# Kernel optimization log

Hardware: AMD Instinct MI355X
Metric: run time of the kernel (lower is better)

## Reference

```python
import jax, jax.numpy as jnp
import numpy as np

D = 768
H = 12
EPS = 1e-5


def layer_norm(x, g, b):
    mu = jnp.mean(x, axis=-1, keepdims=True)
    var = jnp.var(x, axis=-1, keepdims=True)
    return (x - mu) * jax.lax.rsqrt(var + EPS) * g + b


def setup_inputs() -> dict:
    key = jax.random.key(0)
    ks = jax.random.split(key, 12)
    d, h = D, H
    x = jax.random.normal(ks[0], (4, 1024, d), dtype=jnp.float32)
    # attention projections (per-head dim is full d, per the module)
    s_qkv = (6.0 / (d + d * h)) ** 0.5  # xavier-like scale
    Wq = jax.random.uniform(ks[1], (d, d * h), jnp.float32, -s_qkv, s_qkv)
    Wk = jax.random.uniform(ks[2], (d, d * h), jnp.float32, -s_qkv, s_qkv)
    Wv = jax.random.uniform(ks[3], (d, d * h), jnp.float32, -s_qkv, s_qkv)
    Wu = jax.random.uniform(ks[4], (d * h, d), jnp.float32, -s_qkv, s_qkv)
    bu = jnp.zeros((d,), jnp.float32)
    # MLP
    s1 = (6.0 / (d + 4 * d)) ** 0.5
    W1 = jax.random.uniform(ks[5], (d, 4 * d), jnp.float32, -s1, s1)
    b1 = jax.random.normal(ks[6], (4 * d,), jnp.float32) * 1e-6
    W2 = jax.random.uniform(ks[7], (4 * d, d), jnp.float32, -s1, s1)
    b2 = jax.random.normal(ks[8], (d,), jnp.float32) * 1e-6
    ln1_g = jnp.ones((d,), jnp.float32)
    ln1_b = jnp.zeros((d,), jnp.float32)
    ln2_g = jnp.ones((d,), jnp.float32)
    ln2_b = jnp.zeros((d,), jnp.float32)
    return dict(x=x, Wq=Wq, Wk=Wk, Wv=Wv, Wu=Wu, bu=bu,
                ln1_g=ln1_g, ln1_b=ln1_b, ln2_g=ln2_g, ln2_b=ln2_b,
                W1=W1, b1=b1, W2=W2, b2=b2)


def reference(x, Wq, Wk, Wv, Wu, bu, ln1_g, ln1_b, ln2_g, ln2_b, W1, b1, W2, b2):
    b, n, d = x.shape
    h = H
    # --- pre-LN attention block ---
    res = x
    y = layer_norm(x, ln1_g, ln1_b)
    qs = (y @ Wq).reshape(b, n, h, d)  # per-head dim = d (module quirk)
    ks = (y @ Wk).reshape(b, n, h, d)
    vs = (y @ Wv).reshape(b, n, h, d)
    scores = jnp.einsum('bihd,bjhd->bhij', qs, ks) / (d ** 0.5)
    w = jax.nn.softmax(scores, axis=-1)
    att = jnp.einsum('bhij,bjhd->bihd', w, vs).reshape(b, n, h * d)
    y = att @ Wu + bu
    x = y + res
    # --- pre-LN MLP block (dropout is identity at inference) ---
    res = x
    y = layer_norm(x, ln2_g, ln2_b)
    y = jax.nn.relu(y @ W1 + b1)
    y = y @ W2 + b2
    return y + res
```

## Files before the change

kernel.cpp:

```cpp
#include <hip/hip_runtime.h>
#include <cstdint>
#include <cmath>


typedef __bf16 bf16_t;
typedef __bf16 bf16x8 __attribute__((ext_vector_type(8)));
typedef __bf16 bf16x4 __attribute__((ext_vector_type(4)));
typedef float floatx4 __attribute__((ext_vector_type(4)));

#define DMODEL 768
#define NHEAD  12
#define SEQ    1024
#define NBATCH 4
#define ROWS   (NBATCH*SEQ)
#define DH     (DMODEL*NHEAD)
#define DFF    (4*DMODEL)

template<bool BIAS, bool RES, bool RELU, int OMODE>
__global__ __launch_bounds__(256)
void gemm_v7(const bf16_t* __restrict__ A, const bf16_t* __restrict__ BT,
             void* __restrict__ Cv, int K, int lda, int ldb, int ldc,
             int bdiv, long sa_hi, long sa_lo, long sb_hi, long sb_lo,
             long sc_hi, long sc_lo,
             const float* __restrict__ bias, const float* __restrict__ res,
             int ldres, float alpha)
{
  __shared__ __align__(16) bf16_t As[128*64];
  __shared__ __align__(16) bf16_t Bs[128*64];

  const int tid  = threadIdx.x;
  const int wave = tid >> 6;
  const int lane = tid & 63;
  const int r    = lane & 15;
  const int q    = lane >> 4;

  const int z = blockIdx.z;
  A  += (long)(z / bdiv) * sa_hi + (long)(z % bdiv) * sa_lo;
  BT += (long)(z / bdiv) * sb_hi + (long)(z % bdiv) * sb_lo;
  const long coff = (long)(z / bdiv) * sc_hi + (long)(z % bdiv) * sc_lo;

  const int bm = blockIdx.y * 128;
  const int bn = blockIdx.x * 128;
  const int wm = (wave & 1) * 64;
  const int wn = (wave >> 1) * 64;

  const int blk0 = 2*wave, blk1 = 2*wave + 1;
  const bf16_t* a_src0 = A  + (long)(bm + blk0*16 + r) * lda + q*8;
  const bf16_t* a_src1 = A  + (long)(bm + blk1*16 + r) * lda + q*8;
  const bf16_t* b_src0 = BT + (long)(bn + blk0*16 + r) * ldb + q*8;
  const bf16_t* b_src1 = BT + (long)(bn + blk1*16 + r) * ldb + q*8;
  const int da0 = blk0*512 + lane*8;
  const int da1 = blk1*512 + lane*8;

  const int am = (wave & 1) * 4;
  const int bb = (wave >> 1) * 4;

  floatx4 acc[4][4] = {};

  for (int k0 = 0; k0 < K; k0 += 64) {
    bf16x8 a00 = *(const bf16x8*)(a_src0 + k0);
    bf16x8 a01 = *(const bf16x8*)(a_src0 + k0 + 32);
    bf16x8 a10 = *(const bf16x8*)(a_src1 + k0);
    bf16x8 a11 = *(const bf16x8*)(a_src1 + k0 + 32);
    bf16x8 b00 = *(const bf16x8*)(b_src0 + k0);
    bf16x8 b01 = *(const bf16x8*)(b_src0 + k0 + 32);
    bf16x8 b10 = *(const bf16x8*)(b_src1 + k0);
    bf16x8 b11 = *(const bf16x8*)(b_src1 + k0 + 32);
    *(bf16x8*)(As + da0)        = a00;
    *(bf16x8*)(As + 4096 + da0) = a01;
    *(bf16x8*)(As + da1)        = a10;
    *(bf16x8*)(As + 4096 + da1) = a11;
    *(bf16x8*)(Bs + da0)        = b00;
    *(bf16x8*)(Bs + 4096 + da0) = b01;
    *(bf16x8*)(Bs + da1)        = b10;
    *(bf16x8*)(Bs + 4096 + da1) = b11;
    __syncthreads();
#pragma unroll
    for (int p = 0; p < 2; ++p) {
      bf16x8 afrag[4], bfrag[4];
#pragma unroll
      for (int t = 0; t < 4; ++t) {
        afrag[t] = *(const bf16x8*)(As + p*4096 + (am + t)*512 + lane*8);
        bfrag[t] = *(const bf16x8*)(Bs + p*4096 + (bb + t)*512 + lane*8);
      }
#pragma unroll
      for (int mt = 0; mt < 4; ++mt)
#pragma unroll
        for (int nt = 0; nt < 4; ++nt)
          acc[mt][nt] = __builtin_amdgcn_mfma_f32_16x16x32_bf16(
              afrag[mt], bfrag[nt], acc[mt][nt], 0, 0, 0);
    }
    __syncthreads();
  }

  const int row0 = bm + wm + q*4;
  const int col0 = bn + wn + r;
#pragma unroll
  for (int nt = 0; nt < 4; ++nt) {
    const int col = col0 + nt*16;
    float bv = 0.f;
    if (BIAS) bv = bias[col];
#pragma unroll
    for (int mt = 0; mt < 4; ++mt) {
#pragma unroll
      for (int e = 0; e < 4; ++e) {
        const int rowi = row0 + mt*16 + e;
        float v = acc[mt][nt][e] * alpha;
        if (BIAS) v += bv;
        if (RELU) v = fmaxf(v, 0.f);
        if (RES)  v += res[(long)rowi * ldres + col];
        const long idx = coff + (long)rowi * ldc + col;
        if (OMODE == 0)      ((bf16_t*)Cv)[idx] = (bf16_t)v;
        else if (OMODE == 1) ((float*)Cv)[idx] = v;
        else                 ((float*)Cv)[idx] += v;
      }
    }
  }
}

__global__ void tr_f2b_v7(const float* __restrict__ in, bf16_t* __restrict__ out,
                          int ldi, int ldo)
{
  __shared__ bf16_t tile[32][34];
  const int c0 = blockIdx.x * 32, r0 = blockIdx.y * 32;
  const int tx = threadIdx.x, ty = threadIdx.y;
#pragma unroll
  for (int i = 0; i < 4; ++i)
    tile[ty + 8*i][tx] = (bf16_t)in[(long)(r0 + ty + 8*i) * ldi + c0 + tx];
  __syncthreads();
#pragma unroll
  for (int i = 0; i < 4; ++i)
    out[(long)(c0 + ty + 8*i) * ldo + r0 + tx] = tile[tx][ty + 8*i];
}

__global__ void tr_b_v7(const bf16_t* __restrict__ in, bf16_t* __restrict__ out,
                        int ldi, int ldo, int bdiv,
                        long si_hi, long si_lo, long so_hi, long so_lo)
{
  __shared__ bf16_t tile[32][34];
  const int z = blockIdx.z;
  in  += (long)(z / bdiv) * si_hi + (long)(z % bdiv) * si_lo;
  out += (long)(z / bdiv) * so_hi + (long)(z % bdiv) * so_lo;
  const int c0 = blockIdx.x * 32, r0 = blockIdx.y * 32;
  const int tx = threadIdx.x, ty = threadIdx.y;
#pragma unroll
  for (int i = 0; i < 4; ++i)
    tile[ty + 8*i][tx] = in[(long)(r0 + ty + 8*i) * ldi + c0 + tx];
  __syncthreads();
#pragma unroll
  for (int i = 0; i < 4; ++i)
    out[(long)(c0 + ty + 8*i) * ldo + r0 + tx] = tile[tx][ty + 8*i];
}

__global__ void tr_wh_v7(const float* __restrict__ Wq, const float* __restrict__ Wk,
                         const float* __restrict__ Wv, const float* __restrict__ Wu,
                         bf16_t* __restrict__ WhT, bf16_t* __restrict__ WuTh, int h)
{
  __shared__ bf16_t tile[32][34];
  const int z = blockIdx.z;
  const float* in; bf16_t* out; int ldi;
  if (z < 3) {
    const float* W = (z == 0) ? Wq : (z == 1) ? Wk : Wv;
    in  = W + (long)h * DMODEL;
    ldi = DH;
    out = WhT + (long)z * DMODEL * DMODEL;
  } else {
    in  = Wu + (long)h * DMODEL * DMODEL;
    ldi = DMODEL;
    out = WuTh;
  }
  const int c0 = blockIdx.x * 32, r0 = blockIdx.y * 32;
  const int tx = threadIdx.x, ty = threadIdx.y;
#pragma unroll
  for (int i = 0; i < 4; ++i)
    tile[ty + 8*i][tx] = (bf16_t)in[(long)(r0 + ty + 8*i) * ldi + c0 + tx];
  __syncthreads();
#pragma unroll
  for (int i = 0; i < 4; ++i)
    out[(long)(c0 + ty + 8*i) * DMODEL + r0 + tx] = tile[tx][ty + 8*i];
}

__global__ void cast3_v7(const float* __restrict__ a, const float* __restrict__ b,
                         const float* __restrict__ c,
                         bf16_t* __restrict__ oa, bf16_t* __restrict__ ob,
                         bf16_t* __restrict__ oc)
{
  const float* src = (blockIdx.z == 0) ? a : (blockIdx.z == 1) ? b : c;
  bf16_t* dst      = (blockIdx.z == 0) ? oa : (blockIdx.z == 1) ? ob : oc;
  const long i = ((long)blockIdx.x * 256 + threadIdx.x) * 4;
  float4 v = *(const float4*)(src + i);
  bf16x4 o;
  o[0] = (bf16_t)v.x; o[1] = (bf16_t)v.y; o[2] = (bf16_t)v.z; o[3] = (bf16_t)v.w;
  *(bf16x4*)(dst + i) = o;
}

__global__ void cast1_v7(const float* __restrict__ src, bf16_t* __restrict__ dst)
{
  const long i = ((long)blockIdx.x * 256 + threadIdx.x) * 4;
  float4 v = *(const float4*)(src + i);
  bf16x4 o;
  o[0] = (bf16_t)v.x; o[1] = (bf16_t)v.y; o[2] = (bf16_t)v.z; o[3] = (bf16_t)v.w;
  *(bf16x4*)(dst + i) = o;
}

__global__ void ln_v7(const float* __restrict__ x, const float* __restrict__ g,
                      const float* __restrict__ b, bf16_t* __restrict__ y)
{
  const long row = blockIdx.x;
  const int tid = threadIdx.x;
  const float* xr = x + row * DMODEL;
  float v0 = xr[tid], v1 = xr[tid + 256], v2 = xr[tid + 512];
  float s  = v0 + v1 + v2;
  float ss = v0*v0 + v1*v1 + v2*v2;
  for (int o = 32; o; o >>= 1) { s += __shfl_down(s, o); ss += __shfl_down(ss, o); }
  __shared__ float rs[4], rss[4];
  const int wave = tid >> 6, lane = tid & 63;
  if (lane == 0) { rs[wave] = s; rss[wave] = ss; }
  __syncthreads();
  s  = rs[0] + rs[1] + rs[2] + rs[3];
  ss = rss[0] + rss[1] + rss[2] + rss[3];
  const float inv = 1.0f / (float)DMODEL;
  const float mean = s * inv;
  const float var  = ss * inv - mean * mean;
  const float rstd = rsqrtf(var + 1e-5f);
  bf16_t* yr = y + row * DMODEL;
  yr[tid]       = (bf16_t)(((v0 - mean) * rstd) * g[tid]       + b[tid]);
  yr[tid + 256] = (bf16_t)(((v1 - mean) * rstd) * g[tid + 256] + b[tid + 256]);
  yr[tid + 512] = (bf16_t)(((v2 - mean) * rstd) * g[tid + 512] + b[tid + 512]);
}

__global__ void softmax_v7(bf16_t* __restrict__ S)
{
  const long row = blockIdx.x;
  const int tid = threadIdx.x;
  bf16_t* p = S + row * SEQ + tid * 4;
  bf16x4 v = *(const bf16x4*)p;
  float f0 = (float)v[0], f1 = (float)v[1], f2 = (float)v[2], f3 = (float)v[3];
  float m = fmaxf(fmaxf(f0, f1), fmaxf(f2, f3));
  for (int o = 32; o; o >>= 1) m = fmaxf(m, __shfl_down(m, o));
  __shared__ float rm[4], rsum[4];
  const int wave = tid >> 6, lane = tid & 63;
  if (lane == 0) rm[wave] = m;
  __syncthreads();
  m = fmaxf(fmaxf(rm[0], rm[1]), fmaxf(rm[2], rm[3]));
  float e0 = __expf(f0 - m), e1 = __expf(f1 - m), e2 = __expf(f2 - m), e3 = __expf(f3 - m);
  float s = e0 + e1 + e2 + e3;
  for (int o = 32; o; o >>= 1) s += __shfl_down(s, o);
  if (lane == 0) rsum[wave] = s;
  __syncthreads();
  s = rsum[0] + rsum[1] + rsum[2] + rsum[3];
  const float invs = 1.0f / s;
  bf16x4 o4;
  o4[0] = (bf16_t)(e0 * invs); o4[1] = (bf16_t)(e1 * invs);
  o4[2] = (bf16_t)(e2 * invs); o4[3] = (bf16_t)(e3 * invs);
  *(bf16x4*)p = o4;
}

__global__ void finalize_v7(const float* __restrict__ acc, const float* __restrict__ add,
                            const float* __restrict__ bias, float* __restrict__ o)
{
  const long i = (long)blockIdx.x * 256 + threadIdx.x;
  const int c = (int)(i % DMODEL);
  o[i] = acc[i] + bias[c] + add[i];
}

template<int NP>
__global__ void reduce_v7(const float* __restrict__ p, const float* __restrict__ add,
                          const float* __restrict__ bias, float* __restrict__ o,
                          long plane)
{
  const long i = ((long)blockIdx.x * 256 + threadIdx.x) * 4;
  float4 s = *(const float4*)(p + i);
#pragma unroll
  for (int n = 1; n < NP; ++n) {
    float4 v = *(const float4*)(p + i + (long)n * plane);
    s.x += v.x; s.y += v.y; s.z += v.z; s.w += v.w;
  }
  const int c = (int)(i % DMODEL);
  float4 bv = *(const float4*)(bias + c);
  float4 av = *(const float4*)(add + i);
  float4 r;
  r.x = s.x + bv.x + av.x; r.y = s.y + bv.y + av.y;
  r.z = s.z + bv.z + av.z; r.w = s.w + bv.w + av.w;
  *(float4*)(o + i) = r;
}

extern "C" void kernel_launch(void* const* d_in, const int* in_sizes, int n_in,
                              void* d_out, int out_size, void* d_ws, size_t ws_size,
                              hipStream_t stream)
{
  (void)in_sizes; (void)n_in; (void)out_size;
  const float* x    = (const float*)d_in[0];
  const float* Wq   = (const float*)d_in[1];
  const float* Wk   = (const float*)d_in[2];
  const float* Wv   = (const float*)d_in[3];
  const float* Wu   = (const float*)d_in[4];
  const float* bu   = (const float*)d_in[5];
  const float* ln1g = (const float*)d_in[6];
  const float* ln1b = (const float*)d_in[7];
  const float* ln2g = (const float*)d_in[8];
  const float* ln2b = (const float*)d_in[9];
  const float* W1   = (const float*)d_in[10];
  const float* b1   = (const float*)d_in[11];
  const float* W2   = (const float*)d_in[12];
  const float* b2   = (const float*)d_in[13];
  float* out = (float*)d_out;

  char* ws = (char*)d_ws;
  size_t off = 0;
  auto alloc = [&](size_t bytes) -> void* {
    void* p = (void*)(ws + off);
    off += (bytes + 255) & ~(size_t)255;
    return p;
  };

  const float qk_alpha = 1.0f / sqrtf((float)DMODEL);
  dim3 tb(32, 8);

  const size_t SZ_W   = (size_t)DMODEL * DH * 2;
  const size_t SZ_MT  = (size_t)NHEAD * DMODEL * DMODEL * 2;
  const size_t SZ_Y   = (size_t)ROWS * DMODEL * 2;
  const size_t SZ_X2  = (size_t)ROWS * DMODEL * 4;

  if (ws_size >= (size_t)262e6) {
    bf16_t* MT   = (bf16_t*)alloc(SZ_MT);
    bf16_t* PhT  = (bf16_t*)alloc(SZ_MT);
    bf16_t* y    = (bf16_t*)alloc(SZ_Y);
    float*  x2f  = (float* )alloc(SZ_X2);
    float*  part = (float* )alloc((size_t)3 * ROWS * DMODEL * 4);
    bf16_t* S    = (bf16_t*)alloc((size_t)NBATCH * SEQ * NHEAD * SEQ * 2);
    bf16_t* Zt   = (bf16_t*)alloc((size_t)NBATCH * DMODEL * NHEAD * SEQ * 2);
    bf16_t* T_b  = (bf16_t*)part;
    bf16_t* Wqb  = (bf16_t*)S;
    bf16_t* Wkb  = (bf16_t*)((char*)S + SZ_W);
    bf16_t* Wvb  = (bf16_t*)((char*)S + 2*SZ_W);
    bf16_t* WuT  = (bf16_t*)((char*)S + 3*SZ_W);
    bf16_t* W1T  = (bf16_t*)S;
    bf16_t* W2T  = (bf16_t*)((char*)S + 4718592);
    bf16_t* t    = (bf16_t*)((char*)S + 9437184);
    float*  partM= (float* )((char*)S + 34603008);
    bf16_t* y2   = (bf16_t*)Zt;

    cast3_v7<<<dim3(6912, 1, 3), 256, 0, stream>>>(Wq, Wk, Wv, Wqb, Wkb, Wvb);
    tr_f2b_v7<<<dim3(DMODEL/32, DH/32), tb, 0, stream>>>(Wu, WuT, DMODEL, DH);
    gemm_v7<false,false,false,0><<<dim3(6, 6, NHEAD), 256, 0, stream>>>(
        Wkb, Wqb, MT, DMODEL, DH, DH, DMODEL, NHEAD,
        0, DMODEL, 0, DMODEL, 0, (long)DMODEL*DMODEL, nullptr, nullptr, 0, 1.0f);
    gemm_v7<false,false,false,0><<<dim3(6, 6, NHEAD), 256, 0, stream>>>(
        WuT, Wvb, PhT, DMODEL, DH, DH, DMODEL, NHEAD,
        0, DMODEL, 0, DMODEL, 0, (long)DMODEL*DMODEL, nullptr, nullptr, 0, 1.0f);

    ln_v7<<<ROWS, 256, 0, stream>>>(x, ln1g, ln1b, y);
    for (int b = 0; b < NBATCH; ++b) {
      const bf16_t* yb = y + (long)b * SEQ * DMODEL;
      gemm_v7<false,false,false,0><<<dim3(6, 8, NHEAD), 256, 0, stream>>>(
          yb, MT, T_b, DMODEL, DMODEL, DMODEL, DMODEL, NHEAD,
          0, 0, 0, (long)DMODEL*DMODEL, 0, (long)SEQ*DMODEL,
          nullptr, nullptr, 0, 1.0f);
      gemm_v7<false,false,false,0><<<dim3(8, 8, NHEAD), 256, 0, stream>>>(
          T_b, yb, S + (long)b*SEQ*NHEAD*SEQ, DMODEL, DMODEL, DMODEL, NHEAD*SEQ, NHEAD,
          0, (long)SEQ*DMODEL, 0, 0, 0, (long)SEQ,
          nullptr, nullptr, 0, qk_alpha);
    }
    softmax_v7<<<NBATCH*SEQ*NHEAD, 256, 0, stream>>>(S);
    gemm_v7<false,false,false,0><<<dim3(8, 6, NBATCH*NHEAD), 256, 0, stream>>>(
        PhT, y, Zt, DMODEL, DMODEL, DMODEL, NHEAD*SEQ, NHEAD,
        0, (long)DMODEL*DMODEL, (long)SEQ*DMODEL, 0,
        (long)DMODEL*NHEAD*SEQ, (long)SEQ, nullptr, nullptr, 0, 1.0f);
    gemm_v7<false,false,false,1><<<dim3(6, 8, 12), 256, 0, stream>>>(
        S, Zt, part, NHEAD*SEQ/3, NHEAD*SEQ, NHEAD*SEQ, DMODEL, NBATCH,
        (long)(NHEAD*SEQ/3), (long)SEQ*NHEAD*SEQ,
        (long)(NHEAD*SEQ/3), (long)DMODEL*NHEAD*SEQ,
        (long)ROWS*DMODEL, (long)SEQ*DMODEL, nullptr, nullptr, 0, 1.0f);
    reduce_v7<3><<<(ROWS*DMODEL)/1024, 256, 0, stream>>>(
        part, x, bu, x2f, (long)ROWS*DMODEL);

    tr_f2b_v7<<<dim3(DFF/32, DMODEL/32), tb, 0, stream>>>(W1, W1T, DFF, DMODEL);
    tr_f2b_v7<<<dim3(DMODEL/32, DFF/32), tb, 0, stream>>>(W2, W2T, DMODEL, DFF);
    ln_v7<<<ROWS, 256, 0, stream>>>(x2f, ln2g, ln2b, y2);
    gemm_v7<true,false,true,0><<<dim3(DFF/128, ROWS/128, 1), 256, 0, stream>>>(
        y2, W1T, t, DMODEL, DMODEL, DMODEL, DFF, 1, 0,0,0,0,0,0, b1, nullptr, 0, 1.0f);
    gemm_v7<false,false,false,1><<<dim3(6, ROWS/128, 4), 256, 0, stream>>>(
        t, W2T, partM, DFF/4, DFF, DFF, DMODEL, 4,
        0, (long)(DFF/4), 0, (long)(DFF/4), 0, (long)ROWS*DMODEL,
        nullptr, nullptr, 0, 1.0f);
    reduce_v7<4><<<(ROWS*DMODEL)/1024, 256, 0, stream>>>(
        partM, x2f, b2, out, (long)ROWS*DMODEL);
  } else if (ws_size >= (size_t)112e6) {
    bf16_t* MT  = (bf16_t*)alloc(SZ_MT);
    bf16_t* PhT = (bf16_t*)alloc(SZ_MT);
    bf16_t* y   = (bf16_t*)alloc(SZ_Y);
    float*  x2f = (float* )alloc(SZ_X2);
    char*   BIG = (char*  )alloc((size_t)62914560);
    bf16_t* T_b  = (bf16_t*)(BIG);
    bf16_t* S_b  = (bf16_t*)(BIG + 18874368);
    bf16_t* Zt_b = (bf16_t*)(BIG + 44040192);
    float*  part = (float* )(BIG);
    bf16_t* Wqb = (bf16_t*)(BIG);
    bf16_t* Wkb = (bf16_t*)(BIG + SZ_W);
    bf16_t* Wvb = (bf16_t*)(BIG + 2*SZ_W);
    bf16_t* WuT = (bf16_t*)(BIG + 3*SZ_W);
    bf16_t* W1T   = (bf16_t*)(BIG);
    bf16_t* W2T   = (bf16_t*)(BIG + 4718592);
    bf16_t* t     = (bf16_t*)(BIG + 9437184);
    float*  partM = (float* )(BIG + 34603008);
    bf16_t* y2    = y;

    cast3_v7<<<dim3(6912, 1, 3), 256, 0, stream>>>(Wq, Wk, Wv, Wqb, Wkb, Wvb);
    tr_f2b_v7<<<dim3(DMODEL/32, DH/32), tb, 0, stream>>>(Wu, WuT, DMODEL, DH);
    gemm_v7<false,false,false,0><<<dim3(6, 6, NHEAD), 256, 0, stream>>>(
        Wkb, Wqb, MT, DMODEL, DH, DH, DMODEL, NHEAD,
        0, DMODEL, 0, DMODEL, 0, (long)DMODEL*DMODEL, nullptr, nullptr, 0, 1.0f);
    gemm_v7<false,false,false,0><<<dim3(6, 6, NHEAD), 256, 0, stream>>>(
        WuT, Wvb, PhT, DMODEL, DH, DH, DMODEL, NHEAD,
        0, DMODEL, 0, DMODEL, 0, (long)DMODEL*DMODEL, nullptr, nullptr, 0, 1.0f);

    ln_v7<<<ROWS, 256, 0, stream>>>(x, ln1g, ln1b, y);
    for (int b = 0; b < NBATCH; ++b) {
      const bf16_t* yb = y + (long)b * SEQ * DMODEL;
      gemm_v7<false,false,false,0><<<dim3(6, 8, NHEAD), 256, 0, stream>>>(
          yb, MT, T_b, DMODEL, DMODEL, DMODEL, DMODEL, NHEAD,
          0, 0, 0, (long)DMODEL*DMODEL, 0, (long)SEQ*DMODEL,
          nullptr, nullptr, 0, 1.0f);
      gemm_v7<false,false,false,0><<<dim3(8, 8, NHEAD), 256, 0, stream>>>(
          T_b, yb, S_b, DMODEL, DMODEL, DMODEL, NHEAD*SEQ, NHEAD,
          0, (long)SEQ*DMODEL, 0, 0, 0, (long)SEQ,
          nullptr, nullptr, 0, qk_alpha);
      softmax_v7<<<NHEAD*SEQ, 256, 0, stream>>>(S_b);
      gemm_v7<false,false,false,0><<<dim3(8, 6, NHEAD), 256, 0, stream>>>(
          PhT, yb, Zt_b, DMODEL, DMODEL, DMODEL, NHEAD*SEQ, NHEAD,
          0, (long)DMODEL*DMODEL, 0, 0, 0, (long)SEQ,
          nullptr, nullptr, 0, 1.0f);
      gemm_v7<false,false,false,1><<<dim3(6, 8, 6), 256, 0, stream>>>(
          S_b, Zt_b, part, NHEAD*SEQ/6, NHEAD*SEQ, NHEAD*SEQ, DMODEL, 6,
          0, (long)(NHEAD*SEQ/6), 0, (long)(NHEAD*SEQ/6), 0, (long)SEQ*DMODEL,
          nullptr, nullptr, 0, 1.0f);
      reduce_v7<6><<<(SEQ*DMODEL)/1024, 256, 0, stream>>>(
          part, x + (long)b*SEQ*DMODEL, bu, x2f + (long)b*SEQ*DMODEL,
          (long)SEQ*DMODEL);
    }

    tr_f2b_v7<<<dim3(DFF/32, DMODEL/32), tb, 0, stream>>>(W1, W1T, DFF, DMODEL);
    tr_f2b_v7<<<dim3(DMODEL/32, DFF/32), tb, 0, stream>>>(W2, W2T, DMODEL, DFF);
    ln_v7<<<ROWS, 256, 0, stream>>>(x2f, ln2g, ln2b, y2);
    gemm_v7<true,false,true,0><<<dim3(DFF/128, ROWS/128, 1), 256, 0, stream>>>(
        y2, W1T, t, DMODEL, DMODEL, DMODEL, DFF, 1, 0,0,0,0,0,0, b1, nullptr, 0, 1.0f);
    gemm_v7<false,false,false,1><<<dim3(6, ROWS/128, 2), 256, 0, stream>>>(
        t, W2T, partM, DFF/2, DFF, DFF, DMODEL, 2,
        0, (long)(DFF/2), 0, (long)(DFF/2), 0, (long)ROWS*DMODEL,
        nullptr, nullptr, 0, 1.0f);
    reduce_v7<2><<<(ROWS*DMODEL)/1024, 256, 0, stream>>>(
        partM, x2f, b2, out, (long)ROWS*DMODEL);
  } else if (ws_size >= (size_t)70e6) {
    bf16_t* MT  = (bf16_t*)alloc(SZ_MT);
    bf16_t* PhT = (bf16_t*)alloc(SZ_MT);
    bf16_t* y   = (bf16_t*)alloc(SZ_Y);
    char*   R   = (char*  )alloc((size_t)33554432);
    bf16_t* WAb = (bf16_t*)(R);
    bf16_t* WBb = (bf16_t*)(R + SZ_W);
    float*  x2f = (float* )(R);
    bf16_t* T_h = (bf16_t*)(R + 12582912);
    bf16_t* S_h = (bf16_t*)(R + 18874368);
    bf16_t* Z_h = (bf16_t*)(R + 27262976);
    bf16_t* W1T = (bf16_t*)(R + 12582912);
    bf16_t* W2T = (bf16_t*)(R + 17301504);
    bf16_t* t   = (bf16_t*)MT;
    bf16_t* y2  = y;

    cast1_v7<<<6912, 256, 0, stream>>>(Wq, WAb);
    cast1_v7<<<6912, 256, 0, stream>>>(Wk, WBb);
    gemm_v7<false,false,false,0><<<dim3(6, 6, NHEAD), 256, 0, stream>>>(
        WBb, WAb, MT, DMODEL, DH, DH, DMODEL, NHEAD,
        0, DMODEL, 0, DMODEL, 0, (long)DMODEL*DMODEL, nullptr, nullptr, 0, 1.0f);
    cast1_v7<<<6912, 256, 0, stream>>>(Wv, WAb);
    tr_f2b_v7<<<dim3(DMODEL/32, DH/32), tb, 0, stream>>>(Wu, WBb, DMODEL, DH);
    gemm_v7<false,false,false,0><<<dim3(6, 6, NHEAD), 256, 0, stream>>>(
        WBb, WAb, PhT, DMODEL, DH, DH, DMODEL, NHEAD,
        0, DMODEL, 0, DMODEL, 0, (long)DMODEL*DMODEL, nullptr, nullptr, 0, 1.0f);

    ln_v7<<<ROWS, 256, 0, stream>>>(x, ln1g, ln1b, y);
    for (int h = 0; h < NHEAD; ++h) {
      const bf16_t* MTh  = MT  + (long)h * DMODEL * DMODEL;
      const bf16_t* PhTh = PhT + (long)h * DMODEL * DMODEL;
      gemm_v7<false,false,false,0><<<dim3(6, ROWS/128, 1), 256, 0, stream>>>(
          y, MTh, T_h, DMODEL, DMODEL, DMODEL, DMODEL, 1,
          0,0,0,0,0,0, nullptr, nullptr, 0, 1.0f);
      gemm_v7<false,false,false,0><<<dim3(8, 8, NBATCH), 256, 0, stream>>>(
          T_h, y, S_h, DMODEL, DMODEL, DMODEL, SEQ, NBATCH,
          0, (long)SEQ*DMODEL, 0, (long)SEQ*DMODEL, 0, (long)SEQ*SEQ,
          nullptr, nullptr, 0, qk_alpha);
      softmax_v7<<<ROWS, 256, 0, stream>>>(S_h);
      gemm_v7<false,false,false,0><<<dim3(8, 6, NBATCH), 256, 0, stream>>>(
          PhTh, y, Z_h, DMODEL, DMODEL, DMODEL, SEQ, NBATCH,
          0, 0, 0, (long)SEQ*DMODEL, 0, (long)DMODEL*SEQ,
          nullptr, nullptr, 0, 1.0f);
      if (h == 0)
        gemm_v7<false,false,false,1><<<dim3(6, 8, NBATCH), 256, 0, stream>>>(
            S_h, Z_h, x2f, SEQ, SEQ, SEQ, DMODEL, NBATCH,
            0, (long)SEQ*SEQ, 0, (long)DMODEL*SEQ, 0, (long)SEQ*DMODEL,
            nullptr, nullptr, 0, 1.0f);
      else
        gemm_v7<false,false,false,2><<<dim3(6, 8, NBATCH), 256, 0, stream>>>(
            S_h, Z_h, x2f, SEQ, SEQ, SEQ, DMODEL, NBATCH,
            0, (long)SEQ*SEQ, 0, (long)DMODEL*SEQ, 0, (long)SEQ*DMODEL,
            nullptr, nullptr, 0, 1.0f);
    }
    finalize_v7<<<(ROWS*DMODEL)/256, 256, 0, stream>>>(x2f, x, bu, x2f);

    tr_f2b_v7<<<dim3(DFF/32, DMODEL/32), tb, 0, stream>>>(W1, W1T, DFF, DMODEL);
    tr_f2b_v7<<<dim3(DMODEL/32, DFF/32), tb, 0, stream>>>(W2, W2T, DMODEL, DFF);
    ln_v7<<<ROWS, 256, 0, stream>>>(x2f, ln2g, ln2b, y2);
    gemm_v7<true,false,true,0><<<dim3(DFF/128, ROWS/128, 1), 256, 0, stream>>>(
        y2, W1T, t, DMODEL, DMODEL, DMODEL, DFF, 1, 0,0,0,0,0,0, b1, nullptr, 0, 1.0f);
    gemm_v7<true,true,false,1><<<dim3(6, ROWS/128, 1), 256, 0, stream>>>(
        t, W2T, out, DFF/2, DFF, DFF, DMODEL, 1, 0,0,0,0,0,0,
        b2, x2f, DMODEL, 1.0f);
    gemm_v7<false,false,false,2><<<dim3(6, ROWS/128, 1), 256, 0, stream>>>(
        t + DFF/2, W2T + DFF/2, out, DFF/2, DFF, DFF, DMODEL, 1, 0,0,0,0,0,0,
        nullptr, nullptr, 0, 1.0f);
  } else {
    bf16_t* W1T   = (bf16_t*)alloc((size_t)DMODEL * DFF * 2);
    bf16_t* W2T   = (bf16_t*)alloc((size_t)DMODEL * DFF * 2);
    bf16_t* y     = (bf16_t*)alloc(SZ_Y);
    float*  x2f   = (float* )alloc(SZ_X2);
    char*   reg1  = (char*)alloc((size_t)3*DMODEL*DMODEL*2 + (size_t)DMODEL*DMODEL*2 + (size_t)SEQ*DMODEL*2);
    bf16_t* WhT   = (bf16_t*)reg1;
    bf16_t* WuTh  = (bf16_t*)(reg1 + (size_t)3*DMODEL*DMODEL*2);
    bf16_t* attb  = (bf16_t*)(reg1 + (size_t)4*DMODEL*DMODEL*2);
    bf16_t* y2    = (bf16_t*)reg1;
    char*   reg2  = (char*)alloc((size_t)SEQ*3*DMODEL*2 + (size_t)DMODEL*SEQ*2 + (size_t)SEQ*SEQ*2);
    bf16_t* QKVb  = (bf16_t*)reg2;
    bf16_t* Vtb   = (bf16_t*)(reg2 + (size_t)SEQ*3*DMODEL*2);
    bf16_t* Sb    = (bf16_t*)(reg2 + (size_t)SEQ*3*DMODEL*2 + (size_t)DMODEL*SEQ*2);
    bf16_t* tslab = (bf16_t*)reg2;

    tr_f2b_v7<<<dim3(DFF/32, DMODEL/32), tb, 0, stream>>>(W1, W1T, DFF, DMODEL);
    tr_f2b_v7<<<dim3(DMODEL/32, DFF/32), tb, 0, stream>>>(W2, W2T, DMODEL, DFF);
    ln_v7<<<ROWS, 256, 0, stream>>>(x, ln1g, ln1b, y);

    const int N3 = 3 * DMODEL;
    for (int h = 0; h < NHEAD; ++h) {
      tr_wh_v7<<<dim3(24, 24, 4), tb, 0, stream>>>(Wq, Wk, Wv, Wu, WhT, WuTh, h);
      for (int b = 0; b < NBATCH; ++b) {
        const bf16_t* yb = y + (size_t)b * SEQ * DMODEL;
        gemm_v7<false,false,false,0><<<dim3(N3/128, SEQ/128, 1), 256, 0, stream>>>(
            yb, WhT, QKVb, DMODEL, DMODEL, DMODEL, N3, 1, 0,0,0,0,0,0,
            nullptr, nullptr, 0, 1.0f);
        tr_b_v7<<<dim3(DMODEL/32, SEQ/32, 1), tb, 0, stream>>>(
            QKVb + 2*DMODEL, Vtb, N3, SEQ, 1, 0,0,0,0);
        gemm_v7<false,false,false,0><<<dim3(SEQ/128, SEQ/128, 1), 256, 0, stream>>>(
            QKVb, QKVb + DMODEL, Sb, DMODEL, N3, N3, SEQ, 1, 0,0,0,0,0,0,
            nullptr, nullptr, 0, qk_alpha);
        softmax_v7<<<SEQ, 256, 0, stream>>>(Sb);
        gemm_v7<false,false,false,0><<<dim3(DMODEL/128, SEQ/128, 1), 256, 0, stream>>>(
            Sb, Vtb, attb, SEQ, SEQ, SEQ, DMODEL, 1, 0,0,0,0,0,0,
            nullptr, nullptr, 0, 1.0f);
        float* x2b = x2f + (size_t)b * SEQ * DMODEL;
        if (h == 0)
          gemm_v7<false,false,false,1><<<dim3(DMODEL/128, SEQ/128, 1), 256, 0, stream>>>(
              attb, WuTh, x2b, DMODEL, DMODEL, DMODEL, DMODEL, 1, 0,0,0,0,0,0,
              nullptr, nullptr, 0, 1.0f);
        else
          gemm_v7<false,false,false,2><<<dim3(DMODEL/128, SEQ/128, 1), 256, 0, stream>>>(
              attb, WuTh, x2b, DMODEL, DMODEL, DMODEL, DMODEL, 1, 0,0,0,0,0,0,
              nullptr, nullptr, 0, 1.0f);
      }
    }
    finalize_v7<<<(ROWS*DMODEL)/256, 256, 0, stream>>>(x2f, x, bu, x2f);
    ln_v7<<<ROWS, 256, 0, stream>>>(x2f, ln2g, ln2b, y2);
    for (int kb = 0; kb < 4; ++kb) {
      gemm_v7<true,false,true,0><<<dim3(DMODEL/128, ROWS/128, 1), 256, 0, stream>>>(
          y2, W1T + (size_t)kb*DMODEL*DMODEL, tslab, DMODEL, DMODEL, DMODEL, DMODEL, 1,
          0,0,0,0,0,0, b1 + kb*DMODEL, nullptr, 0, 1.0f);
      if (kb == 0)
        gemm_v7<true,true,false,1><<<dim3(DMODEL/128, ROWS/128, 1), 256, 0, stream>>>(
            tslab, W2T + (size_t)kb*DMODEL, out, DMODEL, DMODEL, DFF, DMODEL, 1,
            0,0,0,0,0,0, b2, x2f, DMODEL, 1.0f);
      else
        gemm_v7<false,false,false,2><<<dim3(DMODEL/128, ROWS/128, 1), 256, 0, stream>>>(
            tslab, W2T + (size_t)kb*DMODEL, out, DMODEL, DMODEL, DFF, DMODEL, 1,
            0,0,0,0,0,0, nullptr, nullptr, 0, 1.0f);
    }
  }
}
```

Before: 1.047 ms.

## Use direct global-to-LDS loads, XCD-aware block swizzle, and batch-pair QK launches

Measured after the change: 994.3 us. 5.1% less time.

```diff
diff --git a/kernel.cpp b/kernel.cpp
--- a/kernel.cpp
+++ b/kernel.cpp
@@ -16,9 +16,17 @@
 #define DH     (DMODEL*NHEAD)
 #define DFF    (4*DMODEL)
 
+__device__ __forceinline__ void gload16(const bf16_t* g, bf16_t* l)
+{
+  __builtin_amdgcn_global_load_lds(
+      (const __attribute__((address_space(1))) void*)g,
+      (__attribute__((address_space(3))) void*)l,
+      16, 0, 0);
+}
+
 template<bool BIAS, bool RES, bool RELU, int OMODE>
 __global__ __launch_bounds__(256)
-void gemm_v7(const bf16_t* __restrict__ A, const bf16_t* __restrict__ BT,
+void gemm_v8(const bf16_t* __restrict__ A, const bf16_t* __restrict__ BT,
              void* __restrict__ Cv, int K, int lda, int ldb, int ldc,
              int bdiv, long sa_hi, long sa_lo, long sb_hi, long sb_lo,
              long sc_hi, long sc_lo,
@@ -28,19 +36,28 @@
   __shared__ __align__(16) bf16_t As[128*64];
   __shared__ __align__(16) bf16_t Bs[128*64];
 
+  const long nwg  = (long)gridDim.x * gridDim.y * gridDim.z;
+  const long orig = blockIdx.x + (long)gridDim.x * (blockIdx.y + (long)gridDim.y * blockIdx.z);
+  const long q8 = nwg >> 3, r8 = nwg & 7;
+  const long xcd = orig & 7, loc = orig >> 3;
+  const long swz = (xcd < r8 ? xcd*(q8+1) : r8*(q8+1) + (xcd - r8)*q8) + loc;
+  const int  bix = (int)(swz % (long)gridDim.x);
+  const long rem = swz / (long)gridDim.x;
+  const int  biy = (int)(rem % (long)gridDim.y);
+  const int  biz = (int)(rem / (long)gridDim.y);
+
   const int tid  = threadIdx.x;
   const int wave = tid >> 6;
   const int lane = tid & 63;
   const int r    = lane & 15;
   const int q    = lane >> 4;
 
-  const int z = blockIdx.z;
-  A  += (long)(z / bdiv) * sa_hi + (long)(z % bdiv) * sa_lo;
-  BT += (long)(z / bdiv) * sb_hi + (long)(z % bdiv) * sb_lo;
-  const long coff = (long)(z / bdiv) * sc_hi + (long)(z % bdiv) * sc_lo;
-
-  const int bm = blockIdx.y * 128;
-  const int bn = blockIdx.x * 128;
+  A  += (long)(biz / bdiv) * sa_hi + (long)(biz % bdiv) * sa_lo;
+  BT += (long)(biz / bdiv) * sb_hi + (long)(biz % bdiv) * sb_lo;
+  const long coff = (long)(biz / bdiv) * sc_hi + (long)(biz % bdiv) * sc_lo;
+
+  const int bm = biy * 128;
+  const int bn = bix * 128;
   const int wm = (wave & 1) * 64;
   const int wn = (wave >> 1) * 64;
 
@@ -49,8 +66,10 @@
   const bf16_t* a_src1 = A  + (long)(bm + blk1*16 + r) * lda + q*8;
   const bf16_t* b_src0 = BT + (long)(bn + blk0*16 + r) * ldb + q*8;
   const bf16_t* b_src1 = BT + (long)(bn + blk1*16 + r) * ldb + q*8;
-  const int da0 = blk0*512 + lane*8;
-  const int da1 = blk1*512 + lane*8;
+  bf16_t* a_dst0 = As + blk0*512;
+  bf16_t* a_dst1 = As + blk1*512;
+  bf16_t* b_dst0 = Bs + blk0*512;
+  bf16_t* b_dst1 = Bs + blk1*512;
 
   const int am = (wave & 1) * 4;
   const int bb = (wave >> 1) * 4;
@@ -58,22 +77,14 @@
   floatx4 acc[4][4] = {};
 
   for (int k0 = 0; k0 < K; k0 += 64) {
-    bf16x8 a00 = *(const bf16x8*)(a_src0 + k0);
-    bf16x8 a01 = *(const bf16x8*)(a_src0 + k0 + 32);
-    bf16x8 a10 = *(const bf16x8*)(a_src1 + k0);
-    bf16x8 a11 = *(const bf16x8*)(a_src1 + k0 + 32);
-    bf16x8 b00 = *(const bf16x8*)(b_src0 + k0);
-    bf16x8 b01 = *(const bf16x8*)(b_src0 + k0 + 32);
-    bf16x8 b10 = *(const bf16x8*)(b_src1 + k0);
-    bf16x8 b11 = *(const bf16x8*)(b_src1 + k0 + 32);
-    *(bf16x8*)(As + da0)        = a00;
-    *(bf16x8*)(As + 4096 + da0) = a01;
-    *(bf16x8*)(As + da1)        = a10;
-    *(bf16x8*)(As + 4096 + da1) = a11;
-    *(bf16x8*)(Bs + da0)        = b00;
-    *(bf16x8*)(Bs + 4096 + da0) = b01;
-    *(bf16x8*)(Bs + da1)        = b10;
-    *(bf16x8*)(Bs + 4096 + da1) = b11;
+    gload16(a_src0 + k0,      a_dst0);
+    gload16(a_src1 + k0,      a_dst1);
+    gload16(b_src0 + k0,      b_dst0);
+    gload16(b_src1 + k0,      b_dst1);
+    gload16(a_src0 + k0 + 32, a_dst0 + 4096);
+    gload16(a_src1 + k0 + 32, a_dst1 + 4096);
+    gload16(b_src0 + k0 + 32, b_dst0 + 4096);
+    gload16(b_src1 + k0 + 32, b_dst1 + 4096);
     __syncthreads();
 #pragma unroll
     for (int p = 0; p < 2; ++p) {
@@ -118,7 +129,7 @@
   }
 }
 
-__global__ void tr_f2b_v7(const float* __restrict__ in, bf16_t* __restrict__ out,
+__global__ void tr_f2b_v8(const float* __restrict__ in, bf16_t* __restrict__ out,
                           int ldi, int ldo)
 {
   __shared__ bf16_t tile[32][34];
@@ -133,7 +144,7 @@
     out[(long)(c0 + ty + 8*i) * ldo + r0 + tx] = tile[tx][ty + 8*i];
 }
 
-__global__ void tr_b_v7(const bf16_t* __restrict__ in, bf16_t* __restrict__ out,
+__global__ void tr_b_v8(const bf16_t* __restrict__ in, bf16_t* __restrict__ out,
                         int ldi, int ldo, int bdiv,
                         long si_hi, long si_lo, long so_hi, long so_lo)
 {
@@ -152,7 +163,7 @@
     out[(long)(c0 + ty + 8*i) * ldo + r0 + tx] = tile[tx][ty + 8*i];
 }
 
-__global__ void tr_wh_v7(const float* __restrict__ Wq, const float* __restrict__ Wk,
+__global__ void tr_wh_v8(const float* __restrict__ Wq, const float* __restrict__ Wk,
                          const float* __restrict__ Wv, const float* __restrict__ Wu,
                          bf16_t* __restrict__ WhT, bf16_t* __restrict__ WuTh, int h)
 {
@@ -180,7 +191,7 @@
     out[(long)(c0 + ty + 8*i) * DMODEL + r0 + tx] = tile[tx][ty + 8*i];
 }
 
-__global__ void cast3_v7(const float* __restrict__ a, const float* __restrict__ b,
+__global__ void cast3_v8(const float* __restrict__ a, const float* __restrict__ b,
                          const float* __restrict__ c,
                          bf16_t* __restrict__ oa, bf16_t* __restrict__ ob,
                          bf16_t* __restrict__ oc)
@@ -194,7 +205,7 @@
   *(bf16x4*)(dst + i) = o;
 }
 
-__global__ void cast1_v7(const float* __restrict__ src, bf16_t* __restrict__ dst)
+__global__ void cast1_v8(const float* __restrict__ src, bf16_t* __restrict__ dst)
 {
   const long i = ((long)blockIdx.x * 256 + threadIdx.x) * 4;
   float4 v = *(const float4*)(src + i);
@@ -203,7 +214,7 @@
   *(bf16x4*)(dst + i) = o;
 }
 
-__global__ void ln_v7(const float* __restrict__ x, const float* __restrict__ g,
+__global__ void ln_v8(const float* __restrict__ x, const float* __restrict__ g,
                       const float* __restrict__ b, bf16_t* __restrict__ y)
 {
   const long row = blockIdx.x;
@@ -229,7 +240,7 @@
   yr[tid + 512] = (bf16_t)(((v2 - mean) * rstd) * g[tid + 512] + b[tid + 512]);
 }
 
-__global__ void softmax_v7(bf16_t* __restrict__ S)
+__global__ void softmax_v8(bf16_t* __restrict__ S)
 {
   const long row = blockIdx.x;
   const int tid = threadIdx.x;
@@ -256,7 +267,7 @@
   *(bf16x4*)p = o4;
 }
 
-__global__ void finalize_v7(const float* __restrict__ acc, const float* __restrict__ add,
+__global__ void finalize_v8(const float* __restrict__ acc, const float* __restrict__ add,
                             const float* __restrict__ bias, float* __restrict__ o)
 {
   const long i = (long)blockIdx.x * 256 + threadIdx.x;
@@ -265,7 +276,7 @@
 }
 
 template<int NP>
-__global__ void reduce_v7(const float* __restrict__ p, const float* __restrict__ add,
+__global__ void reduce_v8(const float* __restrict__ p, const float* __restrict__ add,
                           const float* __restrict__ bias, float* __restrict__ o,
                           long plane)
 {
@@ -330,7 +341,7 @@
     float*  part = (float* )alloc((size_t)3 * ROWS * DMODEL * 4);
     bf16_t* S    = (bf16_t*)alloc((size_t)NBATCH * SEQ * NHEAD * SEQ * 2);
     bf16_t* Zt   = (bf16_t*)alloc((size_t)NBATCH * DMODEL * NHEAD * SEQ * 2);
-    bf16_t* T_b  = (bf16_t*)part;
+    bf16_t* T2   = (bf16_t*)part;
     bf16_t* Wqb  = (bf16_t*)S;
     bf16_t* Wkb  = (bf16_t*)((char*)S + SZ_W);
     bf16_t* Wvb  = (bf16_t*)((char*)S + 2*SZ_W);
@@ -341,50 +352,53 @@
     float*  partM= (float* )((char*)S + 34603008);
     bf16_t* y2   = (bf16_t*)Zt;
 
-    cast3_v7<<<dim3(6912, 1, 3), 256, 0, stream>>>(Wq, Wk, Wv, Wqb, Wkb, Wvb);
-    tr_f2b_v7<<<dim3(DMODEL/32, DH/32), tb, 0, stream>>>(Wu, WuT, DMODEL, DH);
-    gemm_v7<false,false,false,0><<<dim3(6, 6, NHEAD), 256, 0, stream>>>(
+    cast3_v8<<<dim3(6912, 1, 3), 256, 0, stream>>>(Wq, Wk, Wv, Wqb, Wkb, Wvb);
+    tr_f2b_v8<<<dim3(DMODEL/32, DH/32), tb, 0, stream>>>(Wu, WuT, DMODEL, DH);
+    gemm_v8<false,false,false,0><<<dim3(6, 6, NHEAD), 256, 0, stream>>>(
         Wkb, Wqb, MT, DMODEL, DH, DH, DMODEL, NHEAD,
         0, DMODEL, 0, DMODEL, 0, (long)DMODEL*DMODEL, nullptr, nullptr, 0, 1.0f);
-    gemm_v7<false,false,false,0><<<dim3(6, 6, NHEAD), 256, 0, stream>>>(
+    gemm_v8<false,false,false,0><<<dim3(6, 6, NHEAD), 256, 0, stream>>>(
         WuT, Wvb, PhT, DMODEL, DH, DH, DMODEL, NHEAD,
         0, DMODEL, 0, DMODEL, 0, (long)DMODEL*DMODEL, nullptr, nullptr, 0, 1.0f);
 
-    ln_v7<<<ROWS, 256, 0, stream>>>(x, ln1g, ln1b, y);
-    for (int b = 0; b < NBATCH; ++b) {
-      const bf16_t* yb = y + (long)b * SEQ * DMODEL;
-      gemm_v7<false,false,false,0><<<dim3(6, 8, NHEAD), 256, 0, stream>>>(
-          yb, MT, T_b, DMODEL, DMODEL, DMODEL, DMODEL, NHEAD,
-          0, 0, 0, (long)DMODEL*DMODEL, 0, (long)SEQ*DMODEL,
+    ln_v8<<<ROWS, 256, 0, stream>>>(x, ln1g, ln1b, y);
+    for (int b0 = 0; b0 < NBATCH; b0 += 2) {
+      const bf16_t* yb = y + (long)b0 * SEQ * DMODEL;
+      gemm_v8<false,false,false,0><<<dim3(6, 8, 2*NHEAD), 256, 0, stream>>>(
+          yb, MT, T2, DMODEL, DMODEL, DMODEL, DMODEL, NHEAD,
+          (long)SEQ*DMODEL, 0, 0, (long)DMODEL*DMODEL,
+          (long)NHEAD*SEQ*DMODEL, (long)SEQ*DMODEL,
           nullptr, nullptr, 0, 1.0f);
-      gemm_v7<false,false,false,0><<<dim3(8, 8, NHEAD), 256, 0, stream>>>(
-          T_b, yb, S + (long)b*SEQ*NHEAD*SEQ, DMODEL, DMODEL, DMODEL, NHEAD*SEQ, NHEAD,
-          0, (long)SEQ*DMODEL, 0, 0, 0, (long)SEQ,
+      gemm_v8<false,false,false,0><<<dim3(8, 8, 2*NHEAD), 256, 0, stream>>>(
+          T2, yb, S + (long)b0*SEQ*NHEAD*SEQ, DMODEL, DMODEL, DMODEL, NHEAD*SEQ, NHEAD,
+          (long)NHEAD*SEQ*DMODEL, (long)SEQ*DMODEL,
+          (long)SEQ*DMODEL, 0,
+          (long)SEQ*NHEAD*SEQ, (long)SEQ,
           nullptr, nullptr, 0, qk_alpha);
     }
-    softmax_v7<<<NBATCH*SEQ*NHEAD, 256, 0, stream>>>(S);
-    gemm_v7<false,false,false,0><<<dim3(8, 6, NBATCH*NHEAD), 256, 0, stream>>>(
+    softmax_v8<<<NBATCH*SEQ*NHEAD, 256, 0, stream>>>(S);
+    gemm_v8<false,false,false,0><<<dim3(8, 6, NBATCH*NHEAD), 256, 0, stream>>>(
         PhT, y, Zt, DMODEL, DMODEL, DMODEL, NHEAD*SEQ, NHEAD,
         0, (long)DMODEL*DMODEL, (long)SEQ*DMODEL, 0,
         (long)DMODEL*NHEAD*SEQ, (long)SEQ, nullptr, nullptr, 0, 1.0f);
-    gemm_v7<false,false,false,1><<<dim3(6, 8, 12), 256, 0, stream>>>(
+    gemm_v8<false,false,false,1><<<dim3(6, 8, 12), 256, 0, stream>>>(
         S, Zt, part, NHEAD*SEQ/3, NHEAD*SEQ, NHEAD*SEQ, DMODEL, NBATCH,
         (long)(NHEAD*SEQ/3), (long)SEQ*NHEAD*SEQ,
         (long)(NHEAD*SEQ/3), (long)DMODEL*NHEAD*SEQ,
         (long)ROWS*DMODEL, (long)SEQ*DMODEL, nullptr, nullptr, 0, 1.0f);
-    reduce_v7<3><<<(ROWS*DMODEL)/1024, 256, 0, stream>>>(
+    reduce_v8<3><<<(ROWS*DMODEL)/1024, 256, 0, stream>>>(
         part, x, bu, x2f, (long)ROWS*DMODEL);
 
-    tr_f2b_v7<<<dim3(DFF/32, DMODEL/32), tb, 0, stream>>>(W1, W1T, DFF, DMODEL);
-    tr_f2b_v7<<<dim3(DMODEL/32, DFF/32), tb, 0, stream>>>(W2, W2T, DMODEL, DFF);
-    ln_v7<<<ROWS, 256, 0, stream>>>(x2f, ln2g, ln2b, y2);
-    gemm_v7<true,false,true,0><<<dim3(DFF/128, ROWS/128, 1), 256, 0, stream>>>(
+    tr_f2b_v8<<<dim3(DFF/32, DMODEL/32), tb, 0, stream>>>(W1, W1T, DFF, DMODEL);
+    tr_f2b_v8<<<dim3(DMODEL/32, DFF/32), tb, 0, stream>>>(W2, W2T, DMODEL, DFF);
+    ln_v8<<<ROWS, 256, 0, stream>>>(x2f, ln2g, ln2b, y2);
+    gemm_v8<true,false,true,0><<<dim3(DFF/128, ROWS/128, 1), 256, 0, stream>>>(
         y2, W1T, t, DMODEL, DMODEL, DMODEL, DFF, 1, 0,0,0,0,0,0, b1, nullptr, 0, 1.0f);
-    gemm_v7<false,false,false,1><<<dim3(6, ROWS/128, 4), 256, 0, stream>>>(
+    gemm_v8<false,false,false,1><<<dim3(6, ROWS/128, 4), 256, 0, stream>>>(
         t, W2T, partM, DFF/4, DFF, DFF, DMODEL, 4,
         0, (long)(DFF/4), 0, (long)(DFF/4), 0, (long)ROWS*DMODEL,
         nullptr, nullptr, 0, 1.0f);
-    reduce_v7<4><<<(ROWS*DMODEL)/1024, 256, 0, stream>>>(
+    reduce_v8<4><<<(ROWS*DMODEL)/1024, 256, 0, stream>>>(
         partM, x2f, b2, out, (long)ROWS*DMODEL);
   } else if (ws_size >= (size_t)112e6) {
     bf16_t* MT  = (bf16_t*)alloc(SZ_MT);
@@ -406,50 +420,50 @@
     float*  partM = (float* )(BIG + 34603008);
     bf16_t* y2    = y;
 
-    cast3_v7<<<dim3(6912, 1, 3), 256, 0, stream>>>(Wq, Wk, Wv, Wqb, Wkb, Wvb);
-    tr_f2b_v7<<<dim3(DMODEL/32, DH/32), tb, 0, stream>>>(Wu, WuT, DMODEL, DH);
-    gemm_v7<false,false,false,0><<<dim3(6, 6, NHEAD), 256, 0, stream>>>(
+    cast3_v8<<<dim3(6912, 1, 3), 256, 0, stream>>>(Wq, Wk, Wv, Wqb, Wkb, Wvb);
+    tr_f2b_v8<<<dim3(DMODEL/32, DH/32), tb, 0, stream>>>(Wu, WuT, DMODEL, DH);
+    gemm_v8<false,false,false,0><<<dim3(6, 6, NHEAD), 256, 0, stream>>>(
         Wkb, Wqb, MT, DMODEL, DH, DH, DMODEL, NHEAD,
         0, DMODEL, 0, DMODEL, 0, (long)DMODEL*DMODEL, nullptr, nullptr, 0, 1.0f);
-    gemm_v7<false,false,false,0><<<dim3(6, 6, NHEAD), 256, 0, stream>>>(
+    gemm_v8<false,false,false,0><<<dim3(6, 6, NHEAD), 256, 0, stream>>>(
         WuT, Wvb, PhT, DMODEL, DH, DH, DMODEL, NHEAD,
         0, DMODEL, 0, DMODEL, 0, (long)DMODEL*DMODEL, nullptr, nullptr, 0, 1.0f);
 
-    ln_v7<<<ROWS, 256, 0, stream>>>(x, ln1g, ln1b, y);
+    ln_v8<<<ROWS, 256, 0, stream>>>(x, ln1g, ln1b, y);
     for (int b = 0; b < NBATCH; ++b) {
       const bf16_t* yb = y + (long)b * SEQ * DMODEL;
-      gemm_v7<false,false,false,0><<<dim3(6, 8, NHEAD), 256, 0, stream>>>(
+      gemm_v8<false,false,false,0><<<dim3(6, 8, NHEAD), 256, 0, stream>>>(
           yb, MT, T_b, DMODEL, DMODEL, DMODEL, DMODEL, NHEAD,
           0, 0, 0, (long)DMODEL*DMODEL, 0, (long)SEQ*DMODEL,
           nullptr, nullptr, 0, 1.0f);
-      gemm_v7<false,false,false,0><<<dim3(8, 8, NHEAD), 256, 0, stream>>>(
+      gemm_v8<false,false,false,0><<<dim3(8, 8, NHEAD), 256, 0, stream>>>(
           T_b, yb, S_b, DMODEL, DMODEL, DMODEL, NHEAD*SEQ, NHEAD,
           0, (long)SEQ*DMODEL, 0, 0, 0, (long)SEQ,
           nullptr, nullptr, 0, qk_alpha);
-      softmax_v7<<<NHEAD*SEQ, 256, 0, stream>>>(S_b);
-      gemm_v7<false,false,false,0><<<dim3(8, 6, NHEAD), 256, 0, stream>>>(
+      softmax_v8<<<NHEAD*SEQ, 256, 0, stream>>>(S_b);
+      gemm_v8<false,false,false,0><<<dim3(8, 6, NHEAD), 256, 0, stream>>>(
           PhT, yb, Zt_b, DMODEL, DMODEL, DMODEL, NHEAD*SEQ, NHEAD,
           0, (long)DMODEL*DMODEL, 0, 0, 0, (long)SEQ,
           nullptr, nullptr, 0, 1.0f);
-      gemm_v7<false,false,false,1><<<dim3(6, 8, 6), 256, 0, stream>>>(
+      gemm_v8<false,false,false,1><<<dim3(6, 8, 6), 256, 0, stream>>>(
           S_b, Zt_b, part, NHEAD*SEQ/6, NHEAD*SEQ, NHEAD*SEQ, DMODEL, 6,
           0, (long)(NHEAD*SEQ/6), 0, (long)(NHEAD*SEQ/6), 0, (long)SEQ*DMODEL,
           nullptr, nullptr, 0, 1.0f);
-      reduce_v7<6><<<(SEQ*DMODEL)/1024, 256, 0, stream>>>(
+      reduce_v8<6><<<(SEQ*DMODEL)/1024, 256, 0, stream>>>(
           part, x + (long)b*SEQ*DMODEL, bu, x2f + (long)b*SEQ*DMODEL,
           (long)SEQ*DMODEL);
     }
 
-    tr_f2b_v7<<<dim3(DFF/32, DMODEL/32), tb, 0, stream>>>(W1, W1T, DFF, DMODEL);
-    tr_f2b_v7<<<dim3(DMODEL/32, DFF/32), tb, 0, stream>>>(W2, W2T, DMODEL, DFF);
-    ln_v7<<<ROWS, 256, 0, stream>>>(x2f, ln2g, ln2b, y2);
-    gemm_v7<true,false,true,0><<<dim3(DFF/128, ROWS/128, 1), 256, 0, stream>>>(
+    tr_f2b_v8<<<dim3(DFF/32, DMODEL/32), tb, 0, stream>>>(W1, W1T, DFF, DMODEL);
+    tr_f2b_v8<<<dim3(DMODEL/32, DFF/32), tb, 0, stream>>>(W2, W2T, DMODEL, DFF);
+    ln_v8<<<ROWS, 256, 0, stream>>>(x2f, ln2g, ln2b, y2);
+    gemm_v8<true,false,true,0><<<dim3(DFF/128, ROWS/128, 1), 256, 0, stream>>>(
         y2, W1T, t, DMODEL, DMODEL, DMODEL, DFF, 1, 0,0,0,0,0,0, b1, nullptr, 0, 1.0f);
-    gemm_v7<false,false,false,1><<<dim3(6, ROWS/128, 2), 256, 0, stream>>>(
+    gemm_v8<false,false,false,1><<<dim3(6, ROWS/128, 2), 256, 0, stream>>>(
         t, W2T, partM, DFF/2, DFF, DFF, DMODEL, 2,
         0, (long)(DFF/2), 0, (long)(DFF/2), 0, (long)ROWS*DMODEL,
         nullptr, nullptr, 0, 1.0f);
-    reduce_v7<2><<<(ROWS*DMODEL)/1024, 256, 0, stream>>>(
+    reduce_v8<2><<<(ROWS*DMODEL)/1024, 256, 0, stream>>>(
         partM, x2f, b2, out, (long)ROWS*DMODEL);
   } else if (ws_size >= (size_t)70e6) {
     bf16_t* MT  = (bf16_t*)alloc(SZ_MT);
@@ -467,55 +481,55 @@
     bf16_t* t   = (bf16_t*)MT;
     bf16_t* y2  = y;
 
-    cast1_v7<<<6912, 256, 0, stream>>>(Wq, WAb);
-    cast1_v7<<<6912, 256, 0, stream>>>(Wk, WBb);
-    gemm_v7<false,false,false,0><<<dim3(6, 6, NHEAD), 256, 0, stream>>>(
+    cast1_v8<<<6912, 256, 0, stream>>>(Wq, WAb);
+    cast1_v8<<<6912, 256, 0, stream>>>(Wk, WBb);
+    gemm_v8<false,false,false,0><<<dim3(6, 6, NHEAD), 256, 0, stream>>>(
         WBb, WAb, MT, DMODEL, DH, DH, DMODEL, NHEAD,
         0, DMODEL, 0, DMODEL, 0, (long)DMODEL*DMODEL, nullptr, nullptr, 0, 1.0f);
-    cast1_v7<<<6912, 256, 0, stream>>>(Wv, WAb);
-    tr_f2b_v7<<<dim3(DMODEL/32, DH/32), tb, 0, stream>>>(Wu, WBb, DMODEL, DH);
-    gemm_v7<false,false,false,0><<<dim3(6, 6, NHEAD), 256, 0, stream>>>(
+    cast1_v8<<<6912, 256, 0, stream>>>(Wv, WAb);
+    tr_f2b_v8<<<dim3(DMODEL/32, DH/32), tb, 0, stream>>>(Wu, WBb, DMODEL, DH);
+    gemm_v8<false,false,false,0><<<dim3(6, 6, NHEAD), 256, 0, stream>>>(
         WBb, WAb, PhT, DMODEL, DH, DH, DMODEL, NHEAD,
         0, DMODEL, 0, DMODEL, 0, (long)DMODEL*DMODEL, nullptr, nullptr, 0, 1.0f);
 
-    ln_v7<<<ROWS, 256, 0, stream>>>(x, ln1g, ln1b, y);
+    ln_v8<<<ROWS, 256, 0, stream>>>(x, ln1g, ln1b, y);
     for (int h = 0; h < NHEAD; ++h) {
       const bf16_t* MTh  = MT  + (long)h * DMODEL * DMODEL;
       const bf16_t* PhTh = PhT + (long)h * DMODEL * DMODEL;
-      gemm_v7<false,false,false,0><<<dim3(6, ROWS/128, 1), 256, 0, stream>>>(
+      gemm_v8<false,false,false,0><<<dim3(6, ROWS/128, 1), 256, 0, stream>>>(
           y, MTh, T_h, DMODEL, DMODEL, DMODEL, DMODEL, 1,
           0,0,0,0,0,0, nullptr, nullptr, 0, 1.0f);
-      gemm_v7<false,false,false,0><<<dim3(8, 8, NBATCH), 256, 0, stream>>>(
+      gemm_v8<false,false,false,0><<<dim3(8, 8, NBATCH), 256, 0, stream>>>(
           T_h, y, S_h, DMODEL, DMODEL, DMODEL, SEQ, NBATCH,
           0, (long)SEQ*DMODEL, 0, (long)SEQ*DMODEL, 0, (long)SEQ*SEQ,
           nullptr, nullptr, 0, qk_alpha);
-      softmax_v7<<<ROWS, 256, 0, stream>>>(S_h);
-      gemm_v7<false,false,false,0><<<dim3(8, 6, NBATCH), 256, 0, stream>>>(
+      softmax_v8<<<ROWS, 256, 0, stream>>>(S_h);
+      gemm_v8<false,false,false,0><<<dim3(8, 6, NBATCH), 256, 0, stream>>>(
           PhTh, y, Z_h, DMODEL, DMODEL, DMODEL, SEQ, NBATCH,
           0, 0, 0, (long)SEQ*DMODEL, 0, (long)DMODEL*SEQ,
           nullptr, nullptr, 0, 1.0f);
       if (h == 0)
-        gemm_v7<false,false,false,1><<<dim3(6, 8, NBATCH), 256, 0, stream>>>(
+        gemm_v8<false,false,false,1><<<dim3(6, 8, NBATCH), 256, 0, stream>>>(
             S_h, Z_h, x2f, SEQ, SEQ, SEQ, DMODEL, NBATCH,
             0, (long)SEQ*SEQ, 0, (long)DMODEL*SEQ, 0, (long)SEQ*DMODEL,
             nullptr, nullptr, 0, 1.0f);
       else
-        gemm_v7<false,false,false,2><<<dim3(6, 8, NBATCH), 256, 0, stream>>>(
+        gemm_v8<false,false,false,2><<<dim3(6, 8, NBATCH), 256, 0, stream>>>(
             S_h, Z_h, x2f, SEQ, SEQ, SEQ, DMODEL, NBATCH,
             0, (long)SEQ*SEQ, 0, (long)DMODEL*SEQ, 0, (long)SEQ*DMODEL,
             nullptr, nullptr, 0, 1.0f);
     }
-    finalize_v7<<<(ROWS*DMODEL)/256, 256, 0, stream>>>(x2f, x, bu, x2f);
-
-    tr_f2b_v7<<<dim3(DFF/32, DMODEL/32), tb, 0, stream>>>(W1, W1T, DFF, DMODEL);
-    tr_f2b_v7<<<dim3(DMODEL/32, DFF/32), tb, 0, stream>>>(W2, W2T, DMODEL, DFF);
-    ln_v7<<<ROWS, 256, 0, stream>>>(x2f, ln2g, ln2b, y2);
-    gemm_v7<true,false,true,0><<<dim3(DFF/128, ROWS/128, 1), 256, 0, stream>>>(
+    finalize_v8<<<(ROWS*DMODEL)/256, 256, 0, stream>>>(x2f, x, bu, x2f);
+
+    tr_f2b_v8<<<dim3(DFF/32, DMODEL/32), tb, 0, stream>>>(W1, W1T, DFF, DMODEL);
+    tr_f2b_v8<<<dim3(DMODEL/32, DFF/32), tb, 0, stream>>>(W2, W2T, DMODEL, DFF);
+    ln_v8<<<ROWS, 256, 0, stream>>>(x2f, ln2g, ln2b, y2);
+    gemm_v8<true,false,true,0><<<dim3(DFF/128, ROWS/128, 1), 256, 0, stream>>>(
         y2, W1T, t, DMODEL, DMODEL, DMODEL, DFF, 1, 0,0,0,0,0,0, b1, nullptr, 0, 1.0f);
-    gemm_v7<true,true,false,1><<<dim3(6, ROWS/128, 1), 256, 0, stream>>>(
+    gemm_v8<true,true,false,1><<<dim3(6, ROWS/128, 1), 256, 0, stream>>>(
         t, W2T, out, DFF/2, DFF, DFF, DMODEL, 1, 0,0,0,0,0,0,
         b2, x2f, DMODEL, 1.0f);
-    gemm_v7<false,false,false,2><<<dim3(6, ROWS/128, 1), 256, 0, stream>>>(
+    gemm_v8<false,false,false,2><<<dim3(6, ROWS/128, 1), 256, 0, stream>>>(
         t + DFF/2, W2T + DFF/2, out, DFF/2, DFF, DFF, DMODEL, 1, 0,0,0,0,0,0,
         nullptr, nullptr, 0, 1.0f);
   } else {
@@ -534,50 +548,50 @@
     bf16_t* Sb    = (bf16_t*)(reg2 + (size_t)SEQ*3*DMODEL*2 + (size_t)DMODEL*SEQ*2);
     bf16_t* tslab = (bf16_t*)reg2;
 
-    tr_f2b_v7<<<dim3(DFF/32, DMODEL/32), tb, 0, stream>>>(W1, W1T, DFF, DMODEL);
-    tr_f2b_v7<<<dim3(DMODEL/32, DFF/32), tb, 0, stream>>>(W2, W2T, DMODEL, DFF);
-    ln_v7<<<ROWS, 256, 0, stream>>>(x, ln1g, ln1b, y);
+    tr_f2b_v8<<<dim3(DFF/32, DMODEL/32), tb, 0, stream>>>(W1, W1T, DFF, DMODEL);
+    tr_f2b_v8<<<dim3(DMODEL/32, DFF/32), tb, 0, stream>>>(W2, W2T, DMODEL, DFF);
+    ln_v8<<<ROWS, 256, 0, stream>>>(x, ln1g, ln1b, y);
 
     const int N3 = 3 * DMODEL;
     for (int h = 0; h < NHEAD; ++h) {
-      tr_wh_v7<<<dim3(24, 24, 4), tb, 0, stream>>>(Wq, Wk, Wv, Wu, WhT, WuTh, h);
+      tr_wh_v8<<<dim3(24, 24, 4), tb, 0, stream>>>(Wq, Wk, Wv, Wu, WhT, WuTh, h);
       for (int b = 0; b < NBATCH; ++b) {
         const bf16_t* yb = y + (size_t)b * SEQ * DMODEL;
-        gemm_v7<false,false,false,0><<<dim3(N3/128, SEQ/128, 1), 256, 0, stream>>>(
+        gemm_v8<false,false,false,0><<<dim3(N3/128, SEQ/128, 1), 256, 0, stream>>>(
             yb, WhT, QKVb, DMODEL, DMODEL, DMODEL, N3, 1, 0,0,0,0,0,0,
             nullptr, nullptr, 0, 1.0f);
-        tr_b_v7<<<dim3(DMODEL/32, SEQ/32, 1), tb, 0, stream>>>(
+        tr_b_v8<<<dim3(DMODEL/32, SEQ/32, 1), tb, 0, stream>>>(
             QKVb + 2*DMODEL, Vtb, N3, SEQ, 1, 0,0,0,0);
-        gemm_v7<false,false,false,0><<<dim3(SEQ/128, SEQ/128, 1), 256, 0, stream>>>(
+        gemm_v8<false,false,false,0><<<dim3(SEQ/128, SEQ/128, 1), 256, 0, stream>>>(
             QKVb, QKVb + DMODEL, Sb, DMODEL, N3, N3, SEQ, 1, 0,0,0,0,0,0,
             nullptr, nullptr, 0, qk_alpha);
-        softmax_v7<<<SEQ, 256, 0, stream>>>(Sb);
-        gemm_v7<false,false,false,0><<<dim3(DMODEL/128, SEQ/128, 1), 256, 0, stream>>>(
+        softmax_v8<<<SEQ, 256, 0, stream>>>(Sb);
+        gemm_v8<false,false,false,0><<<dim3(DMODEL/128, SEQ/128, 1), 256, 0, stream>>>(
             Sb, Vtb, attb, SEQ, SEQ, SEQ, DMODEL, 1, 0,0,0,0,0,0,
             nullptr, nullptr, 0, 1.0f);
         float* x2b = x2f + (size_t)b * SEQ * DMODEL;
         if (h == 0)
-          gemm_v7<false,false,false,1><<<dim3(DMODEL/128, SEQ/128, 1), 256, 0, stream>>>(
+          gemm_v8<false,false,false,1><<<dim3(DMODEL/128, SEQ/128, 1), 256, 0, stream>>>(
               attb, WuTh, x2b, DMODEL, DMODEL, DMODEL, DMODEL, 1, 0,0,0,0,0,0,
               nullptr, nullptr, 0, 1.0f);
         else
-          gemm_v7<false,false,false,2><<<dim3(DMODEL/128, SEQ/128, 1), 256, 0, stream>>>(
+          gemm_v8<false,false,false,2><<<dim3(DMODEL/128, SEQ/128, 1), 256, 0, stream>>>(
               attb, WuTh, x2b, DMODEL, DMODEL, DMODEL, DMODEL, 1, 0,0,0,0,0,0,
               nullptr, nullptr, 0, 1.0f);
       }
     }
-    finalize_v7<<<(ROWS*DMODEL)/256, 256, 0, stream>>>(x2f, x, bu, x2f);
-    ln_v7<<<ROWS, 256, 0, stream>>>(x2f, ln2g, ln2b, y2);
+    finalize_v8<<<(ROWS*DMODEL)/256, 256, 0, stream>>>(x2f, x, bu, x2f);
+    ln_v8<<<ROWS, 256, 0, stream>>>(x2f, ln2g, ln2b, y2);
     for (int kb = 0; kb < 4; ++kb) {
-      gemm_v7<true,false,true,0><<<dim3(DMODEL/128, ROWS/128, 1), 256, 0, stream>>>(
+      gemm_v8<true,false,true,0><<<dim3(DMODEL/128, ROWS/128, 1), 256, 0, stream>>>(
           y2, W1T + (size_t)kb*DMODEL*DMODEL, tslab, DMODEL, DMODEL, DMODEL, DMODEL, 1,
           0,0,0,0,0,0, b1 + kb*DMODEL, nullptr, 0, 1.0f);
       if (kb == 0)
-        gemm_v7<true,true,false,1><<<dim3(DMODEL/128, ROWS/128, 1), 256, 0, stream>>>(
+        gemm_v8<true,true,false,1><<<dim3(DMODEL/128, ROWS/128, 1), 256, 0, stream>>>(
             tslab, W2T + (size_t)kb*DMODEL, out, DMODEL, DMODEL, DFF, DMODEL, 1,
             0,0,0,0,0,0, b2, x2f, DMODEL, 1.0f);
       else
-        gemm_v7<false,false,false,2><<<dim3(DMODEL/128, ROWS/128, 1), 256, 0, stream>>>(
+        gemm_v8<false,false,false,2><<<dim3(DMODEL/128, ROWS/128, 1), 256, 0, stream>>>(
             tslab, W2T + (size_t)kb*DMODEL, out, DMODEL, DMODEL, DFF, DMODEL, 1,
             0,0,0,0,0,0, nullptr, nullptr, 0, 1.0f);
     }
```
